# Kernel tuning notes

Measured on AMD Instinct MI355X. Metric: run time of the kernel, lower is better.

The kernel has to match this reference:

```python
import jax, jax.numpy as jnp
import numpy as np

NUM_CLASSES = 80
ANCHORS = np.array([[10,13],[16,30],[33,23],[30,61],[62,45],[59,119],[116,90],[156,198],[373,326]], np.float32)
MASK = [[0,1,2],[3,4,5],[6,7,8]]
STRIDES = [8, 16, 32]
MAX_OUT = 100      # max_output_size_per_class == max_total_size
IOU_THR = 0.45
SCORE_THR = 0.25
NMS_TOPK = 128     # per-class candidate pre-selection for greedy NMS (>= MAX_OUT)


def setup_inputs() -> dict:
    key = jax.random.key(0)
    k1, k2, k3 = jax.random.split(key, 3)
    B = 16
    C = 3 * (NUM_CLASSES + 5)  # 255
    return {
        'p3': jax.random.normal(k1, (B, 80, 80, C), jnp.float32),
        'p4': jax.random.normal(k2, (B, 40, 40, C), jnp.float32),
        'p5': jax.random.normal(k3, (B, 20, 20, C), jnp.float32),
    }


def _decode(logits, anchors, stride):
    # logits: [B,H,W,3*(nc+5)] -> boxes [B,H*W*3,4] (x1y1x2y2), obj [B,M], cls [B,M,nc]
    B, H, W, _ = logits.shape
    A = anchors.shape[0]
    x = logits.reshape(B, H, W, A, NUM_CLASSES + 5)
    xy = jax.nn.sigmoid(x[..., :2])
    wh_logit = x[..., 2:4]
    obj = jax.nn.sigmoid(x[..., 4])
    cls = jax.nn.sigmoid(x[..., 5:])
    gx, gy = jnp.meshgrid(jnp.arange(W, dtype=x.dtype), jnp.arange(H, dtype=x.dtype))
    grid = jnp.stack([gx, gy], axis=-1)[:, :, None, :]  # [H,W,1,2]
    ctr = (xy + grid) * stride
    wh = jnp.exp(wh_logit) * anchors  # [B,H,W,A,2]
    box = jnp.concatenate([ctr - wh / 2.0, ctr + wh / 2.0], axis=-1)
    return box.reshape(B, -1, 4), obj.reshape(B, -1), cls.reshape(B, -1, NUM_CLASSES)


def _pairwise_iou(b):
    # b: [K,4] x1y1x2y2 -> [K,K]
    area = (b[:, 2] - b[:, 0]) * (b[:, 3] - b[:, 1])
    lt = jnp.maximum(b[:, None, :2], b[None, :, :2])
    rb = jnp.minimum(b[:, None, 2:], b[None, :, 2:])
    wh = jnp.clip(rb - lt, 0.0)
    inter = wh[..., 0] * wh[..., 1]
    return inter / (area[:, None] + area[None, :] - inter + 1e-9)


def _nms_single(boxes, scores):
    # boxes [N,4], scores [N] for one (image, class): greedy NMS on top-K candidates
    s = jnp.where(scores > SCORE_THR, scores, -1.0)
    top_s, idx = jax.lax.top_k(s, NMS_TOPK)   # sorted descending
    b = boxes[idx]                            # [K,4]
    iou = _pairwise_iou(b)                    # [K,K]
    rng = jnp.arange(NMS_TOPK)

    def body(keep, i):
        active = keep[i] & (top_s[i] > 0.0)
        sup = active & (iou[i] > IOU_THR) & (rng > i)
        return keep & ~sup, None

    keep, _ = jax.lax.scan(body, jnp.ones(NMS_TOPK, bool), rng)
    valid = keep & (top_s > 0.0)
    ss = jnp.where(valid, top_s, -1.0)
    sel_s, sel_i = jax.lax.top_k(ss, MAX_OUT)
    return b[sel_i], sel_s                    # [M,4], [M]


def _per_image(boxes, scores_cn):
    # boxes [N,4] shared across classes (q=1), scores_cn [C,N]
    cb, cs = jax.vmap(_nms_single, in_axes=(None, 0))(boxes, scores_cn)  # [C,M,4],[C,M]
    C = cs.shape[0]
    cls_id = jnp.broadcast_to(jnp.arange(C, dtype=boxes.dtype)[:, None], cs.shape)
    fs, fi = jax.lax.top_k(cs.reshape(-1), MAX_OUT)
    fb = cb.reshape(-1, 4)[fi]
    fc = cls_id.reshape(-1)[fi]
    valid = fs > 0.0
    n_valid = jnp.sum(valid).astype(jnp.int32)
    return (jnp.where(valid[:, None], fb, 0.0),
            jnp.where(valid, fs, 0.0),
            jnp.where(valid, fc, 0.0),
            n_valid)


def _forward(p3, p4, p5):
    boxes, objs, clss = [], [], []
    for logits, m, stride in zip((p3, p4, p5), MASK, STRIDES):
        b, o, c = _decode(logits, jnp.asarray(ANCHORS[m]), float(stride))
        boxes.append(b); objs.append(o); clss.append(c)
    boxes = jnp.concatenate(boxes, axis=1)   # [B,N,4]
    obj = jnp.concatenate(objs, axis=1)      # [B,N]
    cls = jnp.concatenate(clss, axis=1)      # [B,N,C]
    scores = obj[..., None] * cls            # [B,N,C]
    return jax.vmap(_per_image)(boxes, scores.transpose(0, 2, 1))


def reference(p3, p4, p5):
    # returns (boxes [B,100,4], scores [B,100], classes [B,100], valid [B])
    return _forward(p3, p4, p5)
```

## Files before the change

kernel.cpp:

```cpp
#include <hip/hip_runtime.h>
#include <stdint.h>

#define NUM_CLASSES 80
#define N_ANCH 25200
#define B_IMG 16
#define NMS_TOPK_ 128
#define MAX_OUT_ 100
#define SCORE_THR_ 0.25f
#define IOU_THR_ 0.45f
#define NBINS 2048
#define CAP 2048
#define CAPB 512
#define CAPC 256
#define TILE_A 80

__constant__ float c_anch[9][2] = {
    {10.f, 13.f}, {16.f, 30.f}, {33.f, 23.f},
    {30.f, 61.f}, {62.f, 45.f}, {59.f, 119.f},
    {116.f, 90.f}, {156.f, 198.f}, {373.f, 326.f}};

__device__ __forceinline__ float sigmoidf_(float x) {
    return 1.0f / (1.0f + expf(-x));
}

__device__ __forceinline__ unsigned int score_bin(unsigned int bits) {
    unsigned int bin = (bits - 0x3E800000u) >> 13;
    if (bin >= NBINS) bin = NBINS - 1;
    return bin;
}


__global__ void __launch_bounds__(256) decode_scores_kernel(
    const float* __restrict__ p3, const float* __restrict__ p4,
    const float* __restrict__ p5, float* __restrict__ boxes,
    float* __restrict__ score_t) {
    int blk = blockIdx.x;
    int b = blk / 315;
    int tile = blk - b * 315;
    const float* p; int W, lvl, il0, base;
    if (tile < 240)      { p = p3; W = 80; lvl = 0; il0 = tile * TILE_A;         base = 0;     }
    else if (tile < 300) { p = p4; W = 40; lvl = 1; il0 = (tile - 240) * TILE_A; base = 19200; }
    else                 { p = p5; W = 20; lvl = 2; il0 = (tile - 300) * TILE_A; base = 24000; }
    float stride = (float)(8 << lvl);

    __shared__ float4 raw4[TILE_A * 85 / 4];
    __shared__ float obj_sh[TILE_A];
    float* raw = (float*)raw4;
    int tid = threadIdx.x;

    const float4* src4 = (const float4*)(p + (size_t)b * ((size_t)W * W * 255) +
                                         (size_t)il0 * 85);
    for (int k = tid; k < TILE_A * 85 / 4; k += 256) raw4[k] = src4[k];
    __syncthreads();

    if (tid < TILE_A) {
        int il = il0 + tid;
        int y = il / (W * 3);
        int t = il - y * (W * 3);
        int x = t / 3;
        int a = t - x * 3;
        const float* q = &raw[tid * 85];
        float cx = (sigmoidf_(q[0]) + (float)x) * stride;
        float cy = (sigmoidf_(q[1]) + (float)y) * stride;
        float bw = expf(q[2]) * c_anch[lvl * 3 + a][0];
        float bh = expf(q[3]) * c_anch[lvl * 3 + a][1];
        int gi = base + il;
        float* bo = boxes + ((size_t)b * N_ANCH + gi) * 4;
        bo[0] = cx - bw * 0.5f; bo[1] = cy - bh * 0.5f;
        bo[2] = cx + bw * 0.5f; bo[3] = cy + bh * 0.5f;
        obj_sh[tid] = sigmoidf_(q[4]);
    }
    __syncthreads();

    int gi0 = base + il0;
    for (int o = tid; o < NUM_CLASSES * (TILE_A / 4); o += 256) {
        int c = o / (TILE_A / 4);
        int q = o - c * (TILE_A / 4);
        int j = q * 4;
        float4 v;
        v.x = obj_sh[j + 0] * sigmoidf_(raw[(j + 0) * 85 + 5 + c]);
        v.y = obj_sh[j + 1] * sigmoidf_(raw[(j + 1) * 85 + 5 + c]);
        v.z = obj_sh[j + 2] * sigmoidf_(raw[(j + 2) * 85 + 5 + c]);
        v.w = obj_sh[j + 3] * sigmoidf_(raw[(j + 3) * 85 + 5 + c]);
        float4* dst = (float4*)(score_t + ((size_t)(b * NUM_CLASSES + c)) * N_ANCH + gi0);
        dst[q] = v;
    }
}

__global__ void __launch_bounds__(256) topk_nms_fast_kernel(
    const float* __restrict__ score_t, const float* __restrict__ boxes,
    float* __restrict__ cls_score, float* __restrict__ cls_box) {
    int b = blockIdx.x / NUM_CLASSES;
    int c = blockIdx.x % NUM_CLASSES;
    int tid = threadIdx.x;
    int lane = tid & 63;
    int wave = tid >> 6;
    const float4* sc4 = (const float4*)(score_t + (size_t)(b * NUM_CLASSES + c) * N_ANCH);

    __shared__ unsigned int hist[NBINS];
    __shared__ unsigned int segsum[256];
    __shared__ unsigned long long sel[CAPB];
    __shared__ float bx[NMS_TOPK_][5];
    __shared__ unsigned int s_cnt;
    __shared__ int s_cut;

    for (int k = tid; k < NBINS; k += 256) hist[k] = 0u;
    if (tid == 0) s_cnt = 0u;
    __syncthreads();

    for (int i = tid; i < N_ANCH / 4; i += 256) {
        float4 v = sc4[i];
        float vv[4] = {v.x, v.y, v.z, v.w};
#pragma unroll
        for (int k = 0; k < 4; ++k) {
            if (vv[k] > SCORE_THR_)
                atomicAdd(&hist[score_bin(__float_as_uint(vv[k]))], 1u);
        }
    }
    __syncthreads();

    unsigned int ss = 0;
    for (int k = 0; k < 8; ++k) ss += hist[tid * 8 + k];
    segsum[tid] = ss;
    __syncthreads();
    if (tid == 0) {
        unsigned int tot = 0; int cut = 0; int t = 255;
        for (; t >= 0; --t) {
            if (tot + segsum[t] >= NMS_TOPK_) break;
            tot += segsum[t];
        }
        if (t >= 0) {
            int j = 7;
            for (; j >= 0; --j) { tot += hist[t * 8 + j]; if (tot >= NMS_TOPK_) break; }
            if (j < 0) j = 0;
            cut = t * 8 + j;
        }
        s_cut = cut;
    }
    __syncthreads();
    unsigned int cutoff = (unsigned int)s_cut;

    for (int i = tid; i < N_ANCH / 4; i += 256) {
        float4 v = sc4[i];
        float vv[4] = {v.x, v.y, v.z, v.w};
#pragma unroll
        for (int k = 0; k < 4; ++k) {
            if (vv[k] > SCORE_THR_) {
                unsigned int bits = __float_as_uint(vv[k]);
                if (score_bin(bits) >= cutoff) {
                    unsigned int pos = atomicAdd(&s_cnt, 1u);
                    if (pos < CAPB) {
                        sel[pos] = ((unsigned long long)bits << 32) |
                                   (unsigned long long)(~(unsigned int)(i * 4 + k));
                    }
                }
            }
        }
    }
    __syncthreads();

    unsigned int M = s_cnt;
    if (M > CAPB) M = CAPB;
    unsigned int P2 = 1;
    while (P2 < M) P2 <<= 1;
    if (P2 < 2) P2 = 2;
    for (unsigned int k = M + tid; k < P2; k += 256) sel[k] = 0ull;
    __syncthreads();

    if (wave == 0) {
        for (unsigned int k = 2; k <= P2; k <<= 1) {
            for (unsigned int j = k >> 1; j > 0; j >>= 1) {
                for (unsigned int t = (unsigned int)lane; t < P2; t += 64) {
                    unsigned int ixj = t ^ j;
                    if (ixj > t) {
                        unsigned long long a0 = sel[t], b0 = sel[ixj];
                        bool desc = ((t & k) == 0);
                        if (desc ? (a0 < b0) : (a0 > b0)) { sel[t] = b0; sel[ixj] = a0; }
                    }
                }
                __threadfence_block();
            }
        }
    }
    __syncthreads();

    unsigned int K = M < NMS_TOPK_ ? M : NMS_TOPK_;
    if (tid < (int)K) {
        unsigned long long kk = sel[tid];
        unsigned int idx = ~((unsigned int)(kk & 0xFFFFFFFFull));
        const float* bp = boxes + ((size_t)b * N_ANCH + idx) * 4;
        bx[tid][0] = bp[0]; bx[tid][1] = bp[1];
        bx[tid][2] = bp[2]; bx[tid][3] = bp[3];
        bx[tid][4] = __uint_as_float((unsigned int)(kk >> 32));
    }
    __syncthreads();

    if (wave == 0) {
        bool k0 = (unsigned int)lane < K;
        bool k1 = (unsigned int)(64 + lane) < K;
        float x00 = 0, y00 = 0, x01 = 0, y01 = 0, a0 = 0, sv0 = 0;
        float x10 = 0, y10 = 0, x11 = 0, y11 = 0, a1 = 0, sv1 = 0;
        if (k0) {
            x00 = bx[lane][0]; y00 = bx[lane][1];
            x01 = bx[lane][2]; y01 = bx[lane][3]; sv0 = bx[lane][4];
            a0 = (x01 - x00) * (y01 - y00);
        }
        if (k1) {
            x10 = bx[64 + lane][0]; y10 = bx[64 + lane][1];
            x11 = bx[64 + lane][2]; y11 = bx[64 + lane][3]; sv1 = bx[64 + lane][4];
            a1 = (x11 - x10) * (y11 - y10);
        }
        unsigned long long km0 = __ballot(k0);
        unsigned long long km1 = __ballot(k1);
        for (unsigned int i = 0; i < K; ++i) {
            bool ki = ((((i < 64) ? km0 : km1) >> (i & 63)) & 1ull) != 0ull;
            if (ki) {
                float rx0 = bx[i][0], ry0 = bx[i][1], rx1 = bx[i][2], ry1 = bx[i][3];
                float ra = (rx1 - rx0) * (ry1 - ry0);
                if (k0 && (unsigned int)lane > i) {
                    float lx = fmaxf(rx0, x00), ly = fmaxf(ry0, y00);
                    float rx = fminf(rx1, x01), ry = fminf(ry1, y01);
                    float w = fmaxf(rx - lx, 0.f), h = fmaxf(ry - ly, 0.f);
                    float inter = w * h;
                    float iou = inter / (ra + a0 - inter + 1e-9f);
                    if (iou > IOU_THR_) k0 = false;
                }
                if (k1 && (unsigned int)(64 + lane) > i) {
                    float lx = fmaxf(rx0, x10), ly = fmaxf(ry0, y10);
                    float rx = fminf(rx1, x11), ry = fminf(ry1, y11);
                    float w = fmaxf(rx - lx, 0.f), h = fmaxf(ry - ly, 0.f);
                    float inter = w * h;
                    float iou = inter / (ra + a1 - inter + 1e-9f);
                    if (iou > IOU_THR_) k1 = false;
                }
                km0 = __ballot(k0);
                km1 = __ballot(k1);
            }
        }
        float* scd = cls_score + ((size_t)b * NUM_CLASSES + c) * MAX_OUT_;
        float* bod = cls_box + ((size_t)b * NUM_CLASSES + c) * (MAX_OUT_ * 4);
        int n0 = __popcll(km0);
        int n = n0 + __popcll(km1);
        if (k0) {
            int pos = __popcll(km0 & ((1ull << lane) - 1ull));
            if (pos < MAX_OUT_) {
                scd[pos] = sv0;
                bod[pos * 4 + 0] = x00; bod[pos * 4 + 1] = y00;
                bod[pos * 4 + 2] = x01; bod[pos * 4 + 3] = y01;
            }
        }
        if (k1) {
            int pos = n0 + __popcll(km1 & ((1ull << lane) - 1ull));
            if (pos < MAX_OUT_) {
                scd[pos] = sv1;
                bod[pos * 4 + 0] = x10; bod[pos * 4 + 1] = y10;
                bod[pos * 4 + 2] = x11; bod[pos * 4 + 3] = y11;
            }
        }
        int start = n < MAX_OUT_ ? n : MAX_OUT_;
        for (int p2 = start + lane; p2 < MAX_OUT_; p2 += 64) {
            scd[p2] = -1.0f;
            bod[p2 * 4 + 0] = 0.f; bod[p2 * 4 + 1] = 0.f;
            bod[p2 * 4 + 2] = 0.f; bod[p2 * 4 + 3] = 0.f;
        }
    }
}

__global__ void __launch_bounds__(256) final_fast_kernel(
    const float* __restrict__ cls_score, const float* __restrict__ cls_box,
    float* __restrict__ out) {
    int b = blockIdx.x;
    int tid = threadIdx.x;
    const int NC = NUM_CLASSES * MAX_OUT_;
    const float* sc = cls_score + (size_t)b * NC;

    __shared__ unsigned int hist[NBINS];
    __shared__ unsigned int segsum[256];
    __shared__ unsigned long long keys[CAPC];
    __shared__ unsigned int s_cnt, s_tot;
    __shared__ int s_cut;

    for (int k = tid; k < NBINS; k += 256) hist[k] = 0u;
    if (tid == 0) s_cnt = 0u;
    __syncthreads();

    for (int k = tid; k < NC; k += 256) {
        float s = sc[k];
        if (s > 0.0f) atomicAdd(&hist[score_bin(__float_as_uint(s))], 1u);
    }
    __syncthreads();

    unsigned int ss = 0;
    for (int k = 0; k < 8; ++k) ss += hist[tid * 8 + k];
    segsum[tid] = ss;
    __syncthreads();
    if (tid == 0) {
        unsigned int total = 0;
        for (int t = 0; t < 256; ++t) total += segsum[t];
        s_tot = total;
        unsigned int tot = 0; int cut = 0; int t = 255;
        for (; t >= 0; --t) {
            if (tot + segsum[t] >= MAX_OUT_) break;
            tot += segsum[t];
        }
        if (t >= 0) {
            int j = 7;
            for (; j >= 0; --j) { tot += hist[t * 8 + j]; if (tot >= MAX_OUT_) break; }
            if (j < 0) j = 0;
            cut = t * 8 + j;
        }
        s_cut = cut;
    }
    __syncthreads();
    unsigned int cutoff = (unsigned int)s_cut;

    for (int k = tid; k < NC; k += 256) {
        float s = sc[k];
        if (s > 0.0f && score_bin(__float_as_uint(s)) >= cutoff) {
            unsigned int pos = atomicAdd(&s_cnt, 1u);
            if (pos < CAPC) {
                keys[pos] = ((unsigned long long)__float_as_uint(s) << 32) |
                            (unsigned long long)(~(unsigned int)k);
            }
        }
    }
    __syncthreads();

    unsigned int M = s_cnt;
    if (M > CAPC) M = CAPC;
    unsigned int P2 = 1;
    while (P2 < M) P2 <<= 1;
    if (P2 < 2) P2 = 2;
    for (unsigned int k = M + tid; k < P2; k += 256) keys[k] = 0ull;
    __syncthreads();

    if (tid < 64) {
        for (unsigned int k = 2; k <= P2; k <<= 1) {
            for (unsigned int j = k >> 1; j > 0; j >>= 1) {
                for (unsigned int t = (unsigned int)tid; t < P2; t += 64) {
                    unsigned int ixj = t ^ j;
                    if (ixj > t) {
                        unsigned long long a0 = keys[t], b0 = keys[ixj];
                        bool desc = ((t & k) == 0);
                        if (desc ? (a0 < b0) : (a0 > b0)) { keys[t] = b0; keys[ixj] = a0; }
                    }
                }
                __threadfence_block();
            }
        }
    }
    __syncthreads();

    float* ob = out;
    float* os = out + B_IMG * MAX_OUT_ * 4;
    float* oc = os + B_IMG * MAX_OUT_;
    float* on = oc + B_IMG * MAX_OUT_;

    unsigned int K = M < MAX_OUT_ ? M : MAX_OUT_;
    if (tid < MAX_OUT_) {
        if ((unsigned int)tid < K) {
            unsigned long long kk = keys[tid];
            unsigned int flat = ~((unsigned int)(kk & 0xFFFFFFFFull));
            float sv = __uint_as_float((unsigned int)(kk >> 32));
            const float* bp = cls_box + ((size_t)b * NC + flat) * 4;
            os[b * MAX_OUT_ + tid] = sv;
            oc[b * MAX_OUT_ + tid] = (float)(flat / MAX_OUT_);
            ob[(b * MAX_OUT_ + tid) * 4 + 0] = bp[0];
            ob[(b * MAX_OUT_ + tid) * 4 + 1] = bp[1];
            ob[(b * MAX_OUT_ + tid) * 4 + 2] = bp[2];
            ob[(b * MAX_OUT_ + tid) * 4 + 3] = bp[3];
        } else {
            os[b * MAX_OUT_ + tid] = 0.0f;
            oc[b * MAX_OUT_ + tid] = 0.0f;
            ob[(b * MAX_OUT_ + tid) * 4 + 0] = 0.0f;
            ob[(b * MAX_OUT_ + tid) * 4 + 1] = 0.0f;
            ob[(b * MAX_OUT_ + tid) * 4 + 2] = 0.0f;
            ob[(b * MAX_OUT_ + tid) * 4 + 3] = 0.0f;
        }
    }
    if (tid == 0) {
        unsigned int nv = s_tot < MAX_OUT_ ? s_tot : MAX_OUT_;
        on[b] = (float)nv;
    }
}


__global__ void __launch_bounds__(256) decode_kernel(
    const float* __restrict__ p3, const float* __restrict__ p4,
    const float* __restrict__ p5, float* __restrict__ boxes,
    float* __restrict__ obj) {
    int gid = blockIdx.x * blockDim.x + threadIdx.x;
    if (gid >= B_IMG * N_ANCH) return;
    int b = gid / N_ANCH;
    int i = gid - b * N_ANCH;
    const float* p; int W, il, lvl; float stride;
    if (i < 19200)      { p = p3; W = 80; il = i;         lvl = 0; stride = 8.f;  }
    else if (i < 24000) { p = p4; W = 40; il = i - 19200; lvl = 1; stride = 16.f; }
    else                { p = p5; W = 20; il = i - 24000; lvl = 2; stride = 32.f; }
    int y = il / (W * 3);
    int t = il - y * W * 3;
    int x = t / 3;
    int a = t - x * 3;
    const float* q = p + ((((size_t)b * W + y) * W + x) * 255 + a * 85);
    float cx = (sigmoidf_(q[0]) + (float)x) * stride;
    float cy = (sigmoidf_(q[1]) + (float)y) * stride;
    float bw = expf(q[2]) * c_anch[lvl * 3 + a][0];
    float bh = expf(q[3]) * c_anch[lvl * 3 + a][1];
    float* bo = boxes + (size_t)gid * 4;
    bo[0] = cx - bw * 0.5f; bo[1] = cy - bh * 0.5f;
    bo[2] = cx + bw * 0.5f; bo[3] = cy + bh * 0.5f;
    obj[gid] = sigmoidf_(q[4]);
}

__device__ __forceinline__ float cand_score(
    const float* __restrict__ p3, const float* __restrict__ p4,
    const float* __restrict__ p5, const float* __restrict__ obj,
    int b, int c, int i) {
    const float* p; int W, il;
    if (i < 19200)      { p = p3; W = 80; il = i;         }
    else if (i < 24000) { p = p4; W = 40; il = i - 19200; }
    else                { p = p5; W = 20; il = i - 24000; }
    int y = il / (W * 3);
    int t = il - y * W * 3;
    int x = t / 3;
    int a = t - x * 3;
    float cl = p[(((size_t)b * W + y) * W + x) * 255 + a * 85 + 5 + c];
    return obj[b * N_ANCH + i] * sigmoidf_(cl);
}

__global__ void __launch_bounds__(256) topk_nms_kernel(
    const float* __restrict__ p3, const float* __restrict__ p4,
    const float* __restrict__ p5, const float* __restrict__ boxes,
    const float* __restrict__ obj, float* __restrict__ cls_score,
    float* __restrict__ cls_box) {
    int b = blockIdx.x / NUM_CLASSES;
    int c = blockIdx.x % NUM_CLASSES;
    int tid = threadIdx.x;

    __shared__ unsigned int hist[NBINS];
    __shared__ unsigned long long keys[CAP];
    __shared__ unsigned int s_cnt, s_cutoff;
    __shared__ float bx[NMS_TOPK_][5];
    __shared__ float bs[NMS_TOPK_];
    __shared__ int keep[NMS_TOPK_];

    for (int k = tid; k < NBINS; k += 256) hist[k] = 0u;
    if (tid == 0) s_cnt = 0u;
    __syncthreads();

    for (int i = tid; i < N_ANCH; i += 256) {
        float s = cand_score(p3, p4, p5, obj, b, c, i);
        if (s > SCORE_THR_) atomicAdd(&hist[score_bin(__float_as_uint(s))], 1u);
    }
    __syncthreads();

    if (tid == 0) {
        unsigned int total = 0;
        int cut = 0;
        for (int k = NBINS - 1; k >= 0; --k) {
            total += hist[k];
            if (total >= NMS_TOPK_) { cut = k; break; }
        }
        s_cutoff = (unsigned int)cut;
    }
    __syncthreads();
    unsigned int cutoff = s_cutoff;

    for (int i = tid; i < N_ANCH; i += 256) {
        float s = cand_score(p3, p4, p5, obj, b, c, i);
        if (s > SCORE_THR_) {
            unsigned int bits = __float_as_uint(s);
            if (score_bin(bits) >= cutoff) {
                unsigned int pos = atomicAdd(&s_cnt, 1u);
                if (pos < CAP) {
                    keys[pos] = ((unsigned long long)bits << 32) |
                                (unsigned long long)(~(unsigned int)i);
                }
            }
        }
    }
    __syncthreads();

    unsigned int M = s_cnt;
    if (M > CAP) M = CAP;
    unsigned int P2 = 1;
    while (P2 < M) P2 <<= 1;
    if (P2 < 2) P2 = 2;
    for (unsigned int k = M + tid; k < P2; k += 256) keys[k] = 0ull;
    __syncthreads();

    for (unsigned int k = 2; k <= P2; k <<= 1) {
        for (unsigned int j = k >> 1; j > 0; j >>= 1) {
            for (unsigned int t = tid; t < P2; t += 256) {
                unsigned int ixj = t ^ j;
                if (ixj > t) {
                    unsigned long long a0 = keys[t], b0 = keys[ixj];
                    bool desc = ((t & k) == 0);
                    if (desc ? (a0 < b0) : (a0 > b0)) { keys[t] = b0; keys[ixj] = a0; }
                }
            }
            __syncthreads();
        }
    }

    unsigned int K = M < NMS_TOPK_ ? M : NMS_TOPK_;
    if (tid < (int)K) {
        unsigned long long kk = keys[tid];
        unsigned int idx = ~((unsigned int)(kk & 0xFFFFFFFFull));
        const float* bp = boxes + ((size_t)b * N_ANCH + idx) * 4;
        bx[tid][0] = bp[0]; bx[tid][1] = bp[1];
        bx[tid][2] = bp[2]; bx[tid][3] = bp[3];
        bs[tid] = __uint_as_float((unsigned int)(kk >> 32));
        keep[tid] = 1;
    }
    __syncthreads();

    for (unsigned int i = 0; i < K; ++i) {
        if (keep[i]) {
            unsigned int t = (unsigned int)tid;
            if (t > i && t < K && keep[t]) {
                float ax0 = bx[i][0], ay0 = bx[i][1], ax1 = bx[i][2], ay1 = bx[i][3];
                float cx0 = bx[t][0], cy0 = bx[t][1], cx1 = bx[t][2], cy1 = bx[t][3];
                float areaA = (ax1 - ax0) * (ay1 - ay0);
                float areaB = (cx1 - cx0) * (cy1 - cy0);
                float lx = fmaxf(ax0, cx0), ly = fmaxf(ay0, cy0);
                float rx = fminf(ax1, cx1), ry = fminf(ay1, cy1);
                float w = rx - lx; if (w < 0.f) w = 0.f;
                float h = ry - ly; if (h < 0.f) h = 0.f;
                float inter = w * h;
                float iou = inter / (areaA + areaB - inter + 1e-9f);
                if (iou > IOU_THR_) keep[t] = 0;
            }
        }
        __syncthreads();
    }

    if (tid == 0) {
        float* scd = cls_score + ((size_t)b * NUM_CLASSES + c) * MAX_OUT_;
        float* bod = cls_box + ((size_t)b * NUM_CLASSES + c) * MAX_OUT_ * 4;
        int out_n = 0;
        for (unsigned int t2 = 0; t2 < K && out_n < MAX_OUT_; ++t2) {
            if (keep[t2]) {
                scd[out_n] = bs[t2];
                bod[out_n * 4 + 0] = bx[t2][0];
                bod[out_n * 4 + 1] = bx[t2][1];
                bod[out_n * 4 + 2] = bx[t2][2];
                bod[out_n * 4 + 3] = bx[t2][3];
                out_n++;
            }
        }
        for (; out_n < MAX_OUT_; ++out_n) {
            scd[out_n] = -1.0f;
            bod[out_n * 4 + 0] = 0.f; bod[out_n * 4 + 1] = 0.f;
            bod[out_n * 4 + 2] = 0.f; bod[out_n * 4 + 3] = 0.f;
        }
    }
}

extern "C" void kernel_launch(void* const* d_in, const int* in_sizes, int n_in,
                              void* d_out, int out_size, void* d_ws, size_t ws_size,
                              hipStream_t stream) {
    const float* p3 = (const float*)d_in[0];
    const float* p4 = (const float*)d_in[1];
    const float* p5 = (const float*)d_in[2];

    const size_t score_t_elems = (size_t)B_IMG * NUM_CLASSES * N_ANCH;
    const size_t boxes_elems   = (size_t)B_IMG * N_ANCH * 4;
    const size_t clsS_elems    = (size_t)B_IMG * NUM_CLASSES * MAX_OUT_;
    const size_t clsB_elems    = clsS_elems * 4;
    const size_t need_fast = (score_t_elems + boxes_elems + clsS_elems + clsB_elems) * sizeof(float);

    float* ws = (float*)d_ws;

    if (ws_size >= need_fast) {
        float* score_t   = ws;
        float* boxes     = score_t + score_t_elems;
        float* cls_score = boxes + boxes_elems;
        float* cls_box   = cls_score + clsS_elems;

        decode_scores_kernel<<<B_IMG * 315, 256, 0, stream>>>(p3, p4, p5, boxes, score_t);
        topk_nms_fast_kernel<<<B_IMG * NUM_CLASSES, 256, 0, stream>>>(
            score_t, boxes, cls_score, cls_box);
        final_fast_kernel<<<B_IMG, 256, 0, stream>>>(cls_score, cls_box, (float*)d_out);
    } else {
        float* boxes = ws;
        float* obj = boxes + boxes_elems;
        float* cls_score = obj + (size_t)B_IMG * N_ANCH;
        float* cls_box = cls_score + clsS_elems;

        int tot = B_IMG * N_ANCH;
        decode_kernel<<<(tot + 255) / 256, 256, 0, stream>>>(p3, p4, p5, boxes, obj);
        topk_nms_kernel<<<B_IMG * NUM_CLASSES, 256, 0, stream>>>(
            p3, p4, p5, boxes, obj, cls_score, cls_box);
        final_fast_kernel<<<B_IMG, 256, 0, stream>>>(cls_score, cls_box, (float*)d_out);
    }
}
```

Baseline: 336.5 us.

## Store class scores as truncated 16-bit keys and recompute exact scores for candidates

The decode kernel now writes each thresholded score as its top 16 bits (zero below threshold), halving the transposed score tensor. The top-k/NMS kernel loads the whole row into registers once, builds a 256-bin histogram directly from the 16-bit values, and reuses those registers for the selection pass instead of rereading global memory. For selected candidates it recomputes the exact float score from the raw logits. The candidate cap grows to 1024 because the coarser bins let more ties through the cutoff. Box writes and reads become float4, and the final kernel stages its per-image scores in shared memory.

```diff
diff --git a/kernel.cpp b/kernel.cpp
--- a/kernel.cpp
+++ b/kernel.cpp
@@ -9,10 +9,13 @@
 #define SCORE_THR_ 0.25f
 #define IOU_THR_ 0.45f
 #define NBINS 2048
+#define NBINS_B 256
 #define CAP 2048
-#define CAPB 512
+#define CAPB 1024
 #define CAPC 256
 #define TILE_A 80
+#define NVEC 3150
+#define NLD 13
 
 __constant__ float c_anch[9][2] = {
     {10.f, 13.f}, {16.f, 30.f}, {33.f, 23.f},
@@ -29,11 +32,26 @@
     return bin;
 }
 
+__device__ __forceinline__ float exact_score(
+    const float* __restrict__ p3, const float* __restrict__ p4,
+    const float* __restrict__ p5, int b, int c, int i) {
+    const float* p; int W, il;
+    if (i < 19200)      { p = p3; W = 80; il = i;         }
+    else if (i < 24000) { p = p4; W = 40; il = i - 19200; }
+    else                { p = p5; W = 20; il = i - 24000; }
+    int y = il / (W * 3);
+    int t = il - y * (W * 3);
+    int x = t / 3;
+    int a = t - x * 3;
+    const float* q = p + ((((size_t)b * W + y) * W + x) * 255 + a * 85);
+    return sigmoidf_(q[4]) * sigmoidf_(q[5 + c]);
+}
+
 
 __global__ void __launch_bounds__(256) decode_scores_kernel(
     const float* __restrict__ p3, const float* __restrict__ p4,
     const float* __restrict__ p5, float* __restrict__ boxes,
-    float* __restrict__ score_t) {
+    unsigned short* __restrict__ score_t) {
     int blk = blockIdx.x;
     int b = blk / 315;
     int tile = blk - b * 315;
@@ -65,93 +83,106 @@
         float bw = expf(q[2]) * c_anch[lvl * 3 + a][0];
         float bh = expf(q[3]) * c_anch[lvl * 3 + a][1];
         int gi = base + il;
-        float* bo = boxes + ((size_t)b * N_ANCH + gi) * 4;
-        bo[0] = cx - bw * 0.5f; bo[1] = cy - bh * 0.5f;
-        bo[2] = cx + bw * 0.5f; bo[3] = cy + bh * 0.5f;
+        float4* bo = (float4*)(boxes + ((size_t)b * N_ANCH + gi) * 4);
+        *bo = make_float4(cx - bw * 0.5f, cy - bh * 0.5f,
+                          cx + bw * 0.5f, cy + bh * 0.5f);
         obj_sh[tid] = sigmoidf_(q[4]);
     }
     __syncthreads();
 
     int gi0 = base + il0;
-    for (int o = tid; o < NUM_CLASSES * (TILE_A / 4); o += 256) {
-        int c = o / (TILE_A / 4);
-        int q = o - c * (TILE_A / 4);
-        int j = q * 4;
-        float4 v;
-        v.x = obj_sh[j + 0] * sigmoidf_(raw[(j + 0) * 85 + 5 + c]);
-        v.y = obj_sh[j + 1] * sigmoidf_(raw[(j + 1) * 85 + 5 + c]);
-        v.z = obj_sh[j + 2] * sigmoidf_(raw[(j + 2) * 85 + 5 + c]);
-        v.w = obj_sh[j + 3] * sigmoidf_(raw[(j + 3) * 85 + 5 + c]);
-        float4* dst = (float4*)(score_t + ((size_t)(b * NUM_CLASSES + c)) * N_ANCH + gi0);
-        dst[q] = v;
+    for (int o = tid; o < NUM_CLASSES * (TILE_A / 8); o += 256) {
+        int c = o / (TILE_A / 8);
+        int q = o - c * (TILE_A / 8);
+        int j = q * 8;
+        unsigned int u[8];
+#pragma unroll
+        for (int k = 0; k < 8; ++k) {
+            float s = obj_sh[j + k] * sigmoidf_(raw[(j + k) * 85 + 5 + c]);
+            u[k] = (s > SCORE_THR_) ? (__float_as_uint(s) >> 16) : 0u;
+        }
+        uint4 w;
+        w.x = u[0] | (u[1] << 16);
+        w.y = u[2] | (u[3] << 16);
+        w.z = u[4] | (u[5] << 16);
+        w.w = u[6] | (u[7] << 16);
+        *(uint4*)(score_t + ((size_t)(b * NUM_CLASSES + c)) * N_ANCH + gi0 + j) = w;
     }
 }
 
 __global__ void __launch_bounds__(256) topk_nms_fast_kernel(
-    const float* __restrict__ score_t, const float* __restrict__ boxes,
+    const float* __restrict__ p3, const float* __restrict__ p4,
+    const float* __restrict__ p5,
+    const unsigned short* __restrict__ score_t, const float* __restrict__ boxes,
     float* __restrict__ cls_score, float* __restrict__ cls_box) {
     int b = blockIdx.x / NUM_CLASSES;
     int c = blockIdx.x % NUM_CLASSES;
     int tid = threadIdx.x;
     int lane = tid & 63;
     int wave = tid >> 6;
-    const float4* sc4 = (const float4*)(score_t + (size_t)(b * NUM_CLASSES + c) * N_ANCH);
-
-    __shared__ unsigned int hist[NBINS];
-    __shared__ unsigned int segsum[256];
+    const uint4* sc8 = (const uint4*)(score_t + (size_t)(b * NUM_CLASSES + c) * N_ANCH);
+
+    __shared__ unsigned int hist[NBINS_B];
     __shared__ unsigned long long sel[CAPB];
     __shared__ float bx[NMS_TOPK_][5];
     __shared__ unsigned int s_cnt;
     __shared__ int s_cut;
 
-    for (int k = tid; k < NBINS; k += 256) hist[k] = 0u;
+    if (tid < NBINS_B) hist[tid] = 0u;
     if (tid == 0) s_cnt = 0u;
     __syncthreads();
 
-    for (int i = tid; i < N_ANCH / 4; i += 256) {
-        float4 v = sc4[i];
-        float vv[4] = {v.x, v.y, v.z, v.w};
-#pragma unroll
-        for (int k = 0; k < 4; ++k) {
-            if (vv[k] > SCORE_THR_)
-                atomicAdd(&hist[score_bin(__float_as_uint(vv[k]))], 1u);
-        }
-    }
-    __syncthreads();
-
-    unsigned int ss = 0;
-    for (int k = 0; k < 8; ++k) ss += hist[tid * 8 + k];
-    segsum[tid] = ss;
-    __syncthreads();
+    uint4 v[NLD];
+    bool val[NLD];
+#pragma unroll
+    for (int j = 0; j < NLD; ++j) {
+        int i = j * 256 + tid;
+        val[j] = (i < NVEC);
+        if (val[j]) v[j] = sc8[i];
+    }
+
+#pragma unroll
+    for (int j = 0; j < NLD; ++j) {
+        if (val[j]) {
+            unsigned int w[4] = {v[j].x, v[j].y, v[j].z, v[j].w};
+#pragma unroll
+            for (int k = 0; k < 4; ++k) {
+                unsigned int lo = w[k] & 0xFFFFu;
+                unsigned int hi = w[k] >> 16;
+                if (lo >= 0x3E80u) atomicAdd(&hist[lo - 0x3E80u], 1u);
+                if (hi >= 0x3E80u) atomicAdd(&hist[hi - 0x3E80u], 1u);
+            }
+        }
+    }
+    __syncthreads();
+
     if (tid == 0) {
-        unsigned int tot = 0; int cut = 0; int t = 255;
-        for (; t >= 0; --t) {
-            if (tot + segsum[t] >= NMS_TOPK_) break;
-            tot += segsum[t];
-        }
-        if (t >= 0) {
-            int j = 7;
-            for (; j >= 0; --j) { tot += hist[t * 8 + j]; if (tot >= NMS_TOPK_) break; }
-            if (j < 0) j = 0;
-            cut = t * 8 + j;
+        unsigned int tot = 0;
+        int cut = 0;
+        for (int k = NBINS_B - 1; k >= 0; --k) {
+            tot += hist[k];
+            if (tot >= NMS_TOPK_) { cut = k; break; }
         }
         s_cut = cut;
     }
     __syncthreads();
-    unsigned int cutoff = (unsigned int)s_cut;
-
-    for (int i = tid; i < N_ANCH / 4; i += 256) {
-        float4 v = sc4[i];
-        float vv[4] = {v.x, v.y, v.z, v.w};
-#pragma unroll
-        for (int k = 0; k < 4; ++k) {
-            if (vv[k] > SCORE_THR_) {
-                unsigned int bits = __float_as_uint(vv[k]);
-                if (score_bin(bits) >= cutoff) {
+    unsigned int ucut = 0x3E80u + (unsigned int)s_cut;
+
+#pragma unroll
+    for (int j = 0; j < NLD; ++j) {
+        if (val[j]) {
+            int i = j * 256 + tid;
+            unsigned int w[4] = {v[j].x, v[j].y, v[j].z, v[j].w};
+#pragma unroll
+            for (int k = 0; k < 8; ++k) {
+                unsigned int u = (k & 1) ? (w[k >> 1] >> 16) : (w[k >> 1] & 0xFFFFu);
+                if (u >= ucut) {
+                    int idx = i * 8 + k;
+                    float s = exact_score(p3, p4, p5, b, c, idx);
                     unsigned int pos = atomicAdd(&s_cnt, 1u);
                     if (pos < CAPB) {
-                        sel[pos] = ((unsigned long long)bits << 32) |
-                                   (unsigned long long)(~(unsigned int)(i * 4 + k));
+                        sel[pos] = ((unsigned long long)__float_as_uint(s) << 32) |
+                                   (unsigned long long)(~(unsigned int)idx);
                     }
                 }
             }
@@ -188,9 +219,9 @@
     if (tid < (int)K) {
         unsigned long long kk = sel[tid];
         unsigned int idx = ~((unsigned int)(kk & 0xFFFFFFFFull));
-        const float* bp = boxes + ((size_t)b * N_ANCH + idx) * 4;
-        bx[tid][0] = bp[0]; bx[tid][1] = bp[1];
-        bx[tid][2] = bp[2]; bx[tid][3] = bp[3];
+        const float4 bp = *(const float4*)(boxes + ((size_t)b * N_ANCH + idx) * 4);
+        bx[tid][0] = bp.x; bx[tid][1] = bp.y;
+        bx[tid][2] = bp.z; bx[tid][3] = bp.w;
         bx[tid][4] = __uint_as_float((unsigned int)(kk >> 32));
     }
     __syncthreads();
@@ -272,20 +303,34 @@
     int b = blockIdx.x;
     int tid = threadIdx.x;
     const int NC = NUM_CLASSES * MAX_OUT_;
-    const float* sc = cls_score + (size_t)b * NC;
-
+    const float4* scin = (const float4*)(cls_score + (size_t)b * NC);
+
+    __shared__ float sc_sh[NUM_CLASSES * MAX_OUT_];
     __shared__ unsigned int hist[NBINS];
     __shared__ unsigned int segsum[256];
     __shared__ unsigned long long keys[CAPC];
     __shared__ unsigned int s_cnt, s_tot;
     __shared__ int s_cut;
 
+    float4 v[8];
+    bool val[8];
+#pragma unroll
+    for (int j = 0; j < 8; ++j) {
+        int i = j * 256 + tid;
+        val[j] = (i < NC / 4);
+        if (val[j]) v[j] = scin[i];
+    }
+#pragma unroll
+    for (int j = 0; j < 8; ++j) {
+        int i = j * 256 + tid;
+        if (val[j]) ((float4*)sc_sh)[i] = v[j];
+    }
     for (int k = tid; k < NBINS; k += 256) hist[k] = 0u;
     if (tid == 0) s_cnt = 0u;
     __syncthreads();
 
     for (int k = tid; k < NC; k += 256) {
-        float s = sc[k];
+        float s = sc_sh[k];
         if (s > 0.0f) atomicAdd(&hist[score_bin(__float_as_uint(s))], 1u);
     }
     __syncthreads();
@@ -315,7 +360,7 @@
     unsigned int cutoff = (unsigned int)s_cut;
 
     for (int k = tid; k < NC; k += 256) {
-        float s = sc[k];
+        float s = sc_sh[k];
         if (s > 0.0f && score_bin(__float_as_uint(s)) >= cutoff) {
             unsigned int pos = atomicAdd(&s_cnt, 1u);
             if (pos < CAPC) {
@@ -412,22 +457,6 @@
     obj[gid] = sigmoidf_(q[4]);
 }
 
-__device__ __forceinline__ float cand_score(
-    const float* __restrict__ p3, const float* __restrict__ p4,
-    const float* __restrict__ p5, const float* __restrict__ obj,
-    int b, int c, int i) {
-    const float* p; int W, il;
-    if (i < 19200)      { p = p3; W = 80; il = i;         }
-    else if (i < 24000) { p = p4; W = 40; il = i - 19200; }
-    else                { p = p5; W = 20; il = i - 24000; }
-    int y = il / (W * 3);
-    int t = il - y * W * 3;
-    int x = t / 3;
-    int a = t - x * 3;
-    float cl = p[(((size_t)b * W + y) * W + x) * 255 + a * 85 + 5 + c];
-    return obj[b * N_ANCH + i] * sigmoidf_(cl);
-}
-
 __global__ void __launch_bounds__(256) topk_nms_kernel(
     const float* __restrict__ p3, const float* __restrict__ p4,
     const float* __restrict__ p5, const float* __restrict__ boxes,
@@ -449,7 +478,7 @@
     __syncthreads();
 
     for (int i = tid; i < N_ANCH; i += 256) {
-        float s = cand_score(p3, p4, p5, obj, b, c, i);
+        float s = exact_score(p3, p4, p5, b, c, i);
         if (s > SCORE_THR_) atomicAdd(&hist[score_bin(__float_as_uint(s))], 1u);
     }
     __syncthreads();
@@ -467,7 +496,7 @@
     unsigned int cutoff = s_cutoff;
 
     for (int i = tid; i < N_ANCH; i += 256) {
-        float s = cand_score(p3, p4, p5, obj, b, c, i);
+        float s = exact_score(p3, p4, p5, b, c, i);
         if (s > SCORE_THR_) {
             unsigned int bits = __float_as_uint(s);
             if (score_bin(bits) >= cutoff) {
@@ -564,26 +593,27 @@
     const float* p4 = (const float*)d_in[1];
     const float* p5 = (const float*)d_in[2];
 
-    const size_t score_t_elems = (size_t)B_IMG * NUM_CLASSES * N_ANCH;
-    const size_t boxes_elems   = (size_t)B_IMG * N_ANCH * 4;
-    const size_t clsS_elems    = (size_t)B_IMG * NUM_CLASSES * MAX_OUT_;
-    const size_t clsB_elems    = clsS_elems * 4;
-    const size_t need_fast = (score_t_elems + boxes_elems + clsS_elems + clsB_elems) * sizeof(float);
-
-    float* ws = (float*)d_ws;
+    const size_t boxes_elems = (size_t)B_IMG * N_ANCH * 4;
+    const size_t scoreU_elems = (size_t)B_IMG * NUM_CLASSES * N_ANCH;
+    const size_t clsS_elems = (size_t)B_IMG * NUM_CLASSES * MAX_OUT_;
+    const size_t clsB_elems = clsS_elems * 4;
+    const size_t need_fast = boxes_elems * 4 + scoreU_elems * 2 +
+                             (clsS_elems + clsB_elems) * 4;
+
+    char* ws = (char*)d_ws;
 
     if (ws_size >= need_fast) {
-        float* score_t   = ws;
-        float* boxes     = score_t + score_t_elems;
-        float* cls_score = boxes + boxes_elems;
-        float* cls_box   = cls_score + clsS_elems;
-
-        decode_scores_kernel<<<B_IMG * 315, 256, 0, stream>>>(p3, p4, p5, boxes, score_t);
+        float* boxes = (float*)ws;
+        unsigned short* score_u = (unsigned short*)(ws + boxes_elems * 4);
+        float* cls_score = (float*)(ws + boxes_elems * 4 + scoreU_elems * 2);
+        float* cls_box = cls_score + clsS_elems;
+
+        decode_scores_kernel<<<B_IMG * 315, 256, 0, stream>>>(p3, p4, p5, boxes, score_u);
         topk_nms_fast_kernel<<<B_IMG * NUM_CLASSES, 256, 0, stream>>>(
-            score_t, boxes, cls_score, cls_box);
+            p3, p4, p5, score_u, boxes, cls_score, cls_box);
         final_fast_kernel<<<B_IMG, 256, 0, stream>>>(cls_score, cls_box, (float*)d_out);
     } else {
-        float* boxes = ws;
+        float* boxes = (float*)ws;
         float* obj = boxes + boxes_elems;
         float* cls_score = obj + (size_t)B_IMG * N_ANCH;
         float* cls_box = cls_score + clsS_elems;
```

Result: slower. 370.4 us (+10.1%).
